# Kernel tuning notes

Hardware: AMD Instinct MI355X
Metric: run time of the kernel (lower is better)

## Reference

```python
import jax, jax.numpy as jnp
import numpy as np

CHEB_K = 3

def setup_inputs() -> dict:
    key = jax.random.key(0)
    ks = jax.random.split(key, 6)
    bs, node, in_dim, out_dim = 8, 1024, 64, 64
    d_e, t_d, embed_dim = 10, 6, 16
    return {
        "x": jax.random.normal(ks[0], (bs, node, in_dim), dtype=jnp.float32),
        "node_emb": jax.random.normal(ks[1], (node, d_e), dtype=jnp.float32),
        "t": jax.random.normal(ks[2], (bs, t_d), dtype=jnp.float32),
        "n_t": jax.random.normal(ks[3], (bs, t_d), dtype=jnp.float32),
        "p": jnp.zeros((1,), dtype=jnp.float32),
        "weights_pool": jax.random.normal(ks[4], (embed_dim, CHEB_K, in_dim, out_dim), dtype=jnp.float32),
        "bias_pool": jax.random.normal(ks[5], (embed_dim, out_dim), dtype=jnp.float32),
    }

def reference(x, node_emb, t, n_t, p, weights_pool, bias_pool):
    # x: [bs, node, in_dim]; node_emb: [node, d_e]; t, n_t: [bs, t_d]
    bs, node, _ = x.shape
    # static adjacency logits shared across batch: [node, node]
    a = node_emb @ node_emb.T
    # temporal scalar per batch: bmm of [bs,1,t_d] x [bs,t_d,1] -> [bs,1,1]
    a_t = jnp.einsum('bd,bd->b', n_t, t)[:, None, None]
    _a = a[None, :, :] + a_t                       # [bs, node, node]
    # period=False branch
    A = jax.nn.softmax(jax.nn.relu(_a), axis=2)    # [bs, node, node]
    # Chebyshev recursion: T0=I, T1=A, Tk = 2A@T_{k-1} - T_{k-2}
    I = jnp.broadcast_to(jnp.eye(node, dtype=x.dtype), (bs, node, node))
    supports = [I, A]
    for _ in range(2, CHEB_K):
        supports.append(jnp.matmul(2.0 * A, supports[-1]) - supports[-2])
    cheb = jnp.stack(supports, axis=1)             # [bs, k, node, node]
    # node+time embedding: [bs, node, d_e + t_d] = [bs, node, embed_dim]
    emb = jnp.concatenate(
        [jnp.broadcast_to(node_emb[None], (bs, node, node_emb.shape[1])),
         jnp.broadcast_to(n_t[:, None, :], (bs, node, n_t.shape[1]))], axis=-1)
    # graph conv: x_g[b,n,k,i] = sum_m cheb[b,k,n,m] x[b,m,i]
    x_g = jnp.einsum('bknm,bmc->bnkc', cheb, x)
    # fuse per-node weight generation into final contraction (same math as
    # weights = einsum('bnd,dkio->bnkio') followed by einsum('bnki,bnkio->bno'))
    out = jnp.einsum('bnki,bnd,dkio->bno', x_g, emb, weights_pool)
    bias = jnp.einsum('bnd,do->bno', emb, bias_pool)
    return out + bias
```

## Files before the change

### kernel.cpp

```cpp
#include <hip/hip_runtime.h>
#include <hip/hip_bf16.h>

#define NODE 1024
#define BS 8
#define XG_K 208

struct alignas(8) bf4 { __hip_bfloat16 a, b, c, d; };
typedef short short8 __attribute__((ext_vector_type(8)));
typedef float f32x16 __attribute__((ext_vector_type(16)));

__global__ __launch_bounds__(256) void k_attn(const float* __restrict__ ne,
                                              const float* __restrict__ t,
                                              const float* __restrict__ nt,
                                              __hip_bfloat16* __restrict__ A16) {
    __shared__ float nel[NODE * 11];
    int tid = threadIdx.x;
    int w = tid >> 6, lane = tid & 63;
    int n = (blockIdx.x << 2) + w;

    for (int i = tid; i < NODE * 10; i += 256) nel[(i / 10) * 11 + (i % 10)] = ne[i];

    float at[8];
#pragma unroll
    for (int b = 0; b < 8; ++b) {
        float s = 0.f;
#pragma unroll
        for (int j = 0; j < 6; ++j) s += nt[b * 6 + j] * t[b * 6 + j];
        at[b] = s;
    }
    __syncthreads();

    float nr[10];
#pragma unroll
    for (int d = 0; d < 10; ++d) nr[d] = nel[n * 11 + d];

    float v[16];
#pragma unroll
    for (int j = 0; j < 16; ++j) {
        const float* row = &nel[(lane + (j << 6)) * 11];
        float s = 0.f;
#pragma unroll
        for (int d = 0; d < 10; ++d) s += nr[d] * row[d];
        v[j] = s;
    }

#pragma unroll
    for (int b = 0; b < 8; ++b) {
        float u[16], s = 0.f;
#pragma unroll
        for (int j = 0; j < 16; ++j) {
            u[j] = __expf(fmaxf(v[j] + at[b], 0.f));
            s += u[j];
        }
#pragma unroll
        for (int off = 32; off > 0; off >>= 1) s += __shfl_xor(s, off);
        float inv = 1.f / s;
        __hip_bfloat16* dst = A16 + (((size_t)(b << 10) + n) << 10);
#pragma unroll
        for (int j = 0; j < 16; ++j) dst[lane + (j << 6)] = __float2bfloat16(u[j] * inv);
    }
}

__global__ __launch_bounds__(256) void k_prepw(const float* __restrict__ x,
                                               const float* __restrict__ W,
                                               const float* __restrict__ bp,
                                               __hip_bfloat16* __restrict__ xT,
                                               __hip_bfloat16* __restrict__ xg,
                                               __hip_bfloat16* __restrict__ wt) {
    __shared__ __hip_bfloat16 sh[64 * XG_K];
    int tid = threadIdx.x;

    if (blockIdx.x < 128) {
        typedef __hip_bfloat16 row72[72];
        row72* T = (row72*)sh;
        int b = blockIdx.x >> 4;
        int n0 = (blockIdx.x & 15) * 64;
        int nloc = tid >> 2, f0 = (tid & 3) * 16;
        size_t row = (size_t)(b << 10) + n0 + nloc;
        {
            const float* src = x + row * 64 + f0;
            __hip_bfloat16* dst = xg + row * XG_K + f0;
#pragma unroll
            for (int j = 0; j < 16; j += 4) {
                float4 vv = *(const float4*)(src + j);
                bf4 o;
                o.a = __float2bfloat16(vv.x); o.b = __float2bfloat16(vv.y);
                o.c = __float2bfloat16(vv.z); o.d = __float2bfloat16(vv.w);
                *(bf4*)(dst + j) = o;
                T[f0 + j][nloc] = o.a; T[f0 + j + 1][nloc] = o.b;
                T[f0 + j + 2][nloc] = o.c; T[f0 + j + 3][nloc] = o.d;
            }
        }
        if (tid < 64) {
            __hip_bfloat16* d2 = xg + ((size_t)(b << 10) + n0 + tid) * XG_K + 192;
            d2[0] = __float2bfloat16(1.0f);
#pragma unroll
            for (int j = 1; j < 16; ++j) d2[j] = __float2bfloat16(0.0f);
        }
        __syncthreads();
        {
            int f = tid >> 2, c0 = (tid & 3) * 16;
            __hip_bfloat16* dst = xT + ((size_t)b * 64 + f) * 1024 + n0 + c0;
#pragma unroll
            for (int j = 0; j < 16; ++j) dst[j] = T[f][c0 + j];
        }
    } else {
        int d = blockIdx.x - 128;
        const float* Wd = W + (size_t)d * 192 * 64;
        for (int i = tid; i < 192 * 64; i += 256) {
            int k = i >> 6, o = i & 63;
            sh[o * XG_K + k] = __float2bfloat16(Wd[i]);
        }
        if (tid < 64) {
            sh[tid * XG_K + 192] = __float2bfloat16(bp[d * 64 + tid]);
#pragma unroll
            for (int j = 1; j < 16; ++j) sh[tid * XG_K + 192 + j] = __float2bfloat16(0.0f);
        }
        __syncthreads();
        __hip_bfloat16* dst = wt + (size_t)d * 64 * XG_K;
        for (int i = tid; i < 64 * XG_K; i += 256) dst[i] = sh[i];
    }
}

#define LOADG(slot, g) do {                                                   \
    const __hip_bfloat16* qa = pa + (g) * 64;                                 \
    const __hip_bfloat16* qb = pb + (g) * 64;                                 \
    as[slot][0] = *(const short8*)(qa);      as[slot][1] = *(const short8*)(qa + 16); \
    as[slot][2] = *(const short8*)(qa + 32); as[slot][3] = *(const short8*)(qa + 48); \
    bs[slot][0] = *(const short8*)(qb);      bs[slot][1] = *(const short8*)(qb + 16); \
    bs[slot][2] = *(const short8*)(qb + 32); bs[slot][3] = *(const short8*)(qb + 48); \
} while (0)

template<bool FIRST>
__global__ __launch_bounds__(256) void k_spmm_mfma(const __hip_bfloat16* __restrict__ A16,
                                                   const __hip_bfloat16* __restrict__ srcT,
                                                   const float* __restrict__ xres,
                                                   __hip_bfloat16* __restrict__ xg,
                                                   __hip_bfloat16* __restrict__ youtT) {
    __shared__ float P[2][32][67];
    int b = blockIdx.x >> 5;
    int n0 = (blockIdx.x & 31) << 5;
    int tid = threadIdx.x;
    int wv = tid >> 6, lane = tid & 63;
    int fh = wv & 1, kh = wv >> 1;
    int l31 = lane & 31, hi = lane >> 5;

    const __hip_bfloat16* pa = srcT + ((size_t)b * 64 + fh * 32 + l31) * 1024 + (kh << 9) + hi * 8;
    const __hip_bfloat16* pb = A16 + ((size_t)b << 20) + (size_t)(n0 + l31) * 1024 + (kh << 9) + hi * 8;

    f32x16 acc0, acc1;
#pragma unroll
    for (int i = 0; i < 16; ++i) { acc0[i] = 0.f; acc1[i] = 0.f; }

    short8 as[3][4], bs[3][4];
    LOADG(0, 0);
    LOADG(1, 1);
#pragma unroll
    for (int g = 0; g < 8; ++g) {
        if (g + 2 < 8) { LOADG((g + 2) % 3, g + 2); }
        int cu = g % 3;
        acc0 = __builtin_amdgcn_mfma_f32_32x32x16_bf16(as[cu][0], bs[cu][0], acc0, 0, 0, 0);
        acc1 = __builtin_amdgcn_mfma_f32_32x32x16_bf16(as[cu][1], bs[cu][1], acc1, 0, 0, 0);
        acc0 = __builtin_amdgcn_mfma_f32_32x32x16_bf16(as[cu][2], bs[cu][2], acc0, 0, 0, 0);
        acc1 = __builtin_amdgcn_mfma_f32_32x32x16_bf16(as[cu][3], bs[cu][3], acc1, 0, 0, 0);
    }
#pragma unroll
    for (int i = 0; i < 16; ++i) acc0[i] += acc1[i];

    if (kh == 1) {
#pragma unroll
        for (int r = 0; r < 16; ++r) {
            int f = hi * 4 + (r >> 2) * 8 + (r & 3);
            P[fh][l31][f] = acc0[r];
        }
    }
    __syncthreads();
    if (kh == 0) {
#pragma unroll
        for (int r = 0; r < 16; ++r) {
            int f = hi * 4 + (r >> 2) * 8 + (r & 3);
            acc0[r] += P[fh][l31][f];
        }

        int node = n0 + l31;
        size_t row = (size_t)(b << 10) + node;
        const int base = FIRST ? 64 : 128;
#pragma unroll
        for (int rg = 0; rg < 4; ++rg) {
            int fb = fh * 32 + hi * 4 + rg * 8;
            float vx = acc0[rg * 4], vy = acc0[rg * 4 + 1];
            float vz = acc0[rg * 4 + 2], vw = acc0[rg * 4 + 3];
            if (!FIRST) {
                float4 xv = *(const float4*)(xres + row * 64 + fb);
                vx = 2.f * vx - xv.x; vy = 2.f * vy - xv.y;
                vz = 2.f * vz - xv.z; vw = 2.f * vw - xv.w;
            }
            bf4 o;
            o.a = __float2bfloat16(vx); o.b = __float2bfloat16(vy);
            o.c = __float2bfloat16(vz); o.d = __float2bfloat16(vw);
            *(bf4*)(xg + row * XG_K + base + fb) = o;
        }
        if (FIRST) {
#pragma unroll
            for (int r = 0; r < 16; ++r) {
                int f = fh * 32 + hi * 4 + (r >> 2) * 8 + (r & 3);
                youtT[((size_t)b * 64 + f) * 1024 + node] = __float2bfloat16(acc0[r]);
            }
        }
    }
}

__global__ __launch_bounds__(512) void k_fuse(const __hip_bfloat16* __restrict__ xg,
                                              const __hip_bfloat16* __restrict__ wt,
                                              const float* __restrict__ ne,
                                              const float* __restrict__ nt,
                                              float* __restrict__ out) {
    __shared__ float P[8][32][67];
    int m0 = blockIdx.x * 32;
    int tid = threadIdx.x;
    int w = tid >> 6;
    int lane = tid & 63;
    int l31 = lane & 31, hi = lane >> 5;
    int b = m0 >> 10;
    int n = (m0 & 1023) + l31;

    int d0 = 2 * w, d1 = 2 * w + 1;
    float e0 = (d0 < 10) ? ne[n * 10 + d0] : nt[b * 6 + (d0 - 10)];
    float e1 = (d1 < 10) ? ne[n * 10 + d1] : nt[b * 6 + (d1 - 10)];

    short8 xf[13];
    const __hip_bfloat16* px = xg + (size_t)(m0 + l31) * XG_K + hi * 8;
#pragma unroll
    for (int k = 0; k < 13; ++k) xf[k] = *(const short8*)(px + k * 16);

    f32x16 z00, z01, z10, z11;
#pragma unroll
    for (int i = 0; i < 16; ++i) { z00[i] = 0.f; z01[i] = 0.f; z10[i] = 0.f; z11[i] = 0.f; }

    const __hip_bfloat16* pw0 = wt + ((size_t)d0 * 64 + l31) * XG_K + hi * 8;
    const __hip_bfloat16* pw1 = pw0 + (size_t)64 * XG_K;
#pragma unroll
    for (int k = 0; k < 13; ++k) {
        short8 a00 = *(const short8*)(pw0 + k * 16);
        short8 a01 = *(const short8*)(pw0 + (size_t)32 * XG_K + k * 16);
        short8 a10 = *(const short8*)(pw1 + k * 16);
        short8 a11 = *(const short8*)(pw1 + (size_t)32 * XG_K + k * 16);
        z00 = __builtin_amdgcn_mfma_f32_32x32x16_bf16(a00, xf[k], z00, 0, 0, 0);
        z01 = __builtin_amdgcn_mfma_f32_32x32x16_bf16(a01, xf[k], z01, 0, 0, 0);
        z10 = __builtin_amdgcn_mfma_f32_32x32x16_bf16(a10, xf[k], z10, 0, 0, 0);
        z11 = __builtin_amdgcn_mfma_f32_32x32x16_bf16(a11, xf[k], z11, 0, 0, 0);
    }

#pragma unroll
    for (int r = 0; r < 16; ++r) {
        int o = (r & 3) + 8 * (r >> 2) + 4 * hi;
        P[w][l31][o]      = e0 * z00[r] + e1 * z10[r];
        P[w][l31][o + 32] = e0 * z01[r] + e1 * z11[r];
    }
    __syncthreads();

    int m = tid >> 4, o0 = (tid & 15) * 4;
    float s0 = 0.f, s1 = 0.f, s2 = 0.f, s3 = 0.f;
#pragma unroll
    for (int ww = 0; ww < 8; ++ww) {
        s0 += P[ww][m][o0];
        s1 += P[ww][m][o0 + 1];
        s2 += P[ww][m][o0 + 2];
        s3 += P[ww][m][o0 + 3];
    }
    *(float4*)(out + (size_t)(m0 + m) * 64 + o0) = make_float4(s0, s1, s2, s3);
}

extern "C" void kernel_launch(void* const* d_in, const int* in_sizes, int n_in,
                              void* d_out, int out_size, void* d_ws, size_t ws_size,
                              hipStream_t stream) {
    const float* x  = (const float*)d_in[0];
    const float* ne = (const float*)d_in[1];
    const float* t  = (const float*)d_in[2];
    const float* nt = (const float*)d_in[3];
    const float* W  = (const float*)d_in[5];
    const float* bp = (const float*)d_in[6];
    float* out = (float*)d_out;

    __hip_bfloat16* wsb = (__hip_bfloat16*)d_ws;
    __hip_bfloat16* A16 = wsb;
    __hip_bfloat16* xT  = wsb + 8388608;
    __hip_bfloat16* y1T = wsb + 8912896;
    __hip_bfloat16* xg  = wsb + 9437184;
    __hip_bfloat16* wt  = wsb + 11141120;

    k_attn<<<NODE / 4, 256, 0, stream>>>(ne, t, nt, A16);
    k_prepw<<<144, 256, 0, stream>>>(x, W, bp, xT, xg, wt);
    k_spmm_mfma<true ><<<BS * 32, 256, 0, stream>>>(A16, xT,  x, xg, y1T);
    k_spmm_mfma<false><<<BS * 32, 256, 0, stream>>>(A16, y1T, x, xg, nullptr);
    k_fuse<<<BS * (NODE / 32), 512, 0, stream>>>(xg, wt, ne, nt, out);
}
```

Measured before the change: 117.2 us.

## Store intermediates in MFMA fragment-major layout for contiguous operand loads

All workspace buffers (attention matrix, transposed x, y1, xg, packed weights) are now written in a fragment-tiled layout. Each wave's short8 MFMA operand loads become fully contiguous 512-byte chunks instead of strided row reads. The attention kernel is reorganized to one batch per block with 512 threads, where each thread computes 64 columns and the row sum is reduced through shared memory. This trades more complex index math and scattered 2-byte y1 stores for coalesced loads in the GEMM kernels.

Result: slower. 123.4 us (+5.3%).

```diff
diff --git a/kernel.cpp b/kernel.cpp
--- a/kernel.cpp
+++ b/kernel.cpp
@@ -3,150 +3,187 @@
 
 #define NODE 1024
 #define BS 8
-#define XG_K 208
 
 struct alignas(8) bf4 { __hip_bfloat16 a, b, c, d; };
 typedef short short8 __attribute__((ext_vector_type(8)));
 typedef float f32x16 __attribute__((ext_vector_type(16)));
 
-__global__ __launch_bounds__(256) void k_attn(const float* __restrict__ ne,
+__device__ __forceinline__ short bf16bits(float f) {
+    __hip_bfloat16 h = __float2bfloat16(f);
+    return *reinterpret_cast<short*>(&h);
+}
+__device__ __forceinline__ float bitstofl(short s) {
+    unsigned u = ((unsigned)(unsigned short)s) << 16;
+    return __uint_as_float(u);
+}
+
+
+__global__ __launch_bounds__(512) void k_attn(const float* __restrict__ ne,
                                               const float* __restrict__ t,
                                               const float* __restrict__ nt,
-                                              __hip_bfloat16* __restrict__ A16) {
+                                              __hip_bfloat16* __restrict__ A16f) {
     __shared__ float nel[NODE * 11];
+    __shared__ float ssum[8][32];
     int tid = threadIdx.x;
     int w = tid >> 6, lane = tid & 63;
-    int n = (blockIdx.x << 2) + w;
-
-    for (int i = tid; i < NODE * 10; i += 256) nel[(i / 10) * 11 + (i % 10)] = ne[i];
-
-    float at[8];
-#pragma unroll
-    for (int b = 0; b < 8; ++b) {
+    int l31 = lane & 31, hi = lane >> 5;
+    int bidx = blockIdx.x;
+    int b = bidx >> 5;
+    int n = (bidx & 31) * 32 + l31;
+
+    for (int i = tid; i < NODE * 10; i += 512) nel[(i / 10) * 11 + (i % 10)] = ne[i];
+
+    float at = 0.f;
+#pragma unroll
+    for (int j = 0; j < 6; ++j) at += nt[b * 6 + j] * t[b * 6 + j];
+    __syncthreads();
+
+    float nr[10];
+#pragma unroll
+    for (int d = 0; d < 10; ++d) nr[d] = nel[n * 11 + d];
+
+    int mbase = w * 128 + hi * 64;
+    float z[64];
+#pragma unroll
+    for (int m = 0; m < 64; ++m) {
+        const float* row = &nel[(mbase + m) * 11];
         float s = 0.f;
 #pragma unroll
-        for (int j = 0; j < 6; ++j) s += nt[b * 6 + j] * t[b * 6 + j];
-        at[b] = s;
-    }
+        for (int d = 0; d < 10; ++d) s += nr[d] * row[d];
+        z[m] = s;
+    }
+
+    short8 u16[8];
+    float s = 0.f;
+#pragma unroll
+    for (int c = 0; c < 8; ++c) {
+        short8 pk;
+#pragma unroll
+        for (int j = 0; j < 8; ++j) {
+            float u = __expf(fmaxf(z[c * 8 + j] + at, 0.f));
+            s += u;
+            pk[j] = bf16bits(u);
+        }
+        u16[c] = pk;
+    }
+    s += __shfl_xor(s, 32);
+    if (hi == 0) ssum[w][l31] = s;
     __syncthreads();
-
-    float nr[10];
-#pragma unroll
-    for (int d = 0; d < 10; ++d) nr[d] = nel[n * 11 + d];
-
-    float v[16];
-#pragma unroll
-    for (int j = 0; j < 16; ++j) {
-        const float* row = &nel[(lane + (j << 6)) * 11];
-        float s = 0.f;
-#pragma unroll
-        for (int d = 0; d < 10; ++d) s += nr[d] * row[d];
-        v[j] = s;
-    }
-
-#pragma unroll
-    for (int b = 0; b < 8; ++b) {
-        float u[16], s = 0.f;
-#pragma unroll
-        for (int j = 0; j < 16; ++j) {
-            u[j] = __expf(fmaxf(v[j] + at[b], 0.f));
-            s += u[j];
-        }
-#pragma unroll
-        for (int off = 32; off > 0; off >>= 1) s += __shfl_xor(s, off);
-        float inv = 1.f / s;
-        __hip_bfloat16* dst = A16 + (((size_t)(b << 10) + n) << 10);
-#pragma unroll
-        for (int j = 0; j < 16; ++j) dst[lane + (j << 6)] = __float2bfloat16(u[j] * inv);
+    float tot = 0.f;
+#pragma unroll
+    for (int ww = 0; ww < 8; ++ww) tot += ssum[ww][l31];
+    float inv = 1.f / tot;
+
+    __hip_bfloat16* base = A16f + ((size_t)(bidx * 64 + w * 8 + hi * 4) * 2) * 256 + l31 * 8;
+#pragma unroll
+    for (int c = 0; c < 8; ++c) {
+        short8 pk = u16[c];
+        short8 o;
+#pragma unroll
+        for (int j = 0; j < 8; ++j) o[j] = bf16bits(bitstofl(pk[j]) * inv);
+        *(short8*)(base + c * 256) = o;
     }
 }
 
 __global__ __launch_bounds__(256) void k_prepw(const float* __restrict__ x,
                                                const float* __restrict__ W,
                                                const float* __restrict__ bp,
-                                               __hip_bfloat16* __restrict__ xT,
-                                               __hip_bfloat16* __restrict__ xg,
-                                               __hip_bfloat16* __restrict__ wt) {
-    __shared__ __hip_bfloat16 sh[64 * XG_K];
+                                               __hip_bfloat16* __restrict__ xTf,
+                                               __hip_bfloat16* __restrict__ xgf,
+                                               __hip_bfloat16* __restrict__ wtf) {
     int tid = threadIdx.x;
-
     if (blockIdx.x < 128) {
-        typedef __hip_bfloat16 row72[72];
-        row72* T = (row72*)sh;
+        __shared__ __hip_bfloat16 T[64][72];
         int b = blockIdx.x >> 4;
         int n0 = (blockIdx.x & 15) * 64;
-        int nloc = tid >> 2, f0 = (tid & 3) * 16;
-        size_t row = (size_t)(b << 10) + n0 + nloc;
-        {
-            const float* src = x + row * 64 + f0;
-            __hip_bfloat16* dst = xg + row * XG_K + f0;
-#pragma unroll
-            for (int j = 0; j < 16; j += 4) {
-                float4 vv = *(const float4*)(src + j);
-                bf4 o;
-                o.a = __float2bfloat16(vv.x); o.b = __float2bfloat16(vv.y);
-                o.c = __float2bfloat16(vv.z); o.d = __float2bfloat16(vv.w);
-                *(bf4*)(dst + j) = o;
-                T[f0 + j][nloc] = o.a; T[f0 + j + 1][nloc] = o.b;
-                T[f0 + j + 2][nloc] = o.c; T[f0 + j + 3][nloc] = o.d;
-            }
-        }
-        if (tid < 64) {
-            __hip_bfloat16* d2 = xg + ((size_t)(b << 10) + n0 + tid) * XG_K + 192;
-            d2[0] = __float2bfloat16(1.0f);
-#pragma unroll
-            for (int j = 1; j < 16; ++j) d2[j] = __float2bfloat16(0.0f);
+#pragma unroll
+        for (int it = 0; it < 2; ++it) {
+            int i = it * 256 + tid;
+            int l31 = i & 31, hi2 = (i >> 5) & 1, ks = (i >> 6) & 3, rt = i >> 8;
+            int node = n0 + rt * 32 + l31;
+            const float* src = x + ((size_t)b * 1024 + node) * 64 + ks * 16 + hi2 * 8;
+            short8 o;
+#pragma unroll
+            for (int j = 0; j < 8; ++j) o[j] = bf16bits(src[j]);
+            size_t rtg = (size_t)b * 32 + (n0 >> 5) + rt;
+            *(short8*)(xgf + (rtg * 13 + ks) * 512 + hi2 * 256 + l31 * 8) = o;
+#pragma unroll
+            for (int j = 0; j < 8; ++j) {
+                __hip_bfloat16 h;
+                *reinterpret_cast<short*>(&h) = o[j];
+                T[ks * 16 + hi2 * 8 + j][rt * 32 + l31] = h;
+            }
+        }
+        for (int i = tid; i < 1024; i += 256) {
+            int rt = i >> 9, e = i & 511;
+            size_t rtg = (size_t)b * 32 + (n0 >> 5) + rt;
+            float val = ((e & 7) == 0 && e < 256) ? 1.0f : 0.0f;
+            xgf[(rtg * 13 + 12) * 512 + e] = __float2bfloat16(val);
         }
         __syncthreads();
-        {
-            int f = tid >> 2, c0 = (tid & 3) * 16;
-            __hip_bfloat16* dst = xT + ((size_t)b * 64 + f) * 1024 + n0 + c0;
-#pragma unroll
-            for (int j = 0; j < 16; ++j) dst[j] = T[f][c0 + j];
+#pragma unroll
+        for (int fh = 0; fh < 2; ++fh) {
+            int f = fh * 32 + (tid & 31);
+            int m8 = tid >> 5;
+            int m = n0 + m8 * 8;
+            short8 o;
+#pragma unroll
+            for (int j = 0; j < 8; ++j) {
+                __hip_bfloat16 h = T[f][m8 * 8 + j];
+                o[j] = *reinterpret_cast<short*>(&h);
+            }
+            size_t addr = (((size_t)(b * 2 + fh) * 64 + (m >> 4)) * 2 + ((m >> 3) & 1)) * 256 + (f & 31) * 8;
+            *(short8*)(xTf + addr) = o;
         }
     } else {
         int d = blockIdx.x - 128;
         const float* Wd = W + (size_t)d * 192 * 64;
-        for (int i = tid; i < 192 * 64; i += 256) {
-            int k = i >> 6, o = i & 63;
-            sh[o * XG_K + k] = __float2bfloat16(Wd[i]);
-        }
-        if (tid < 64) {
-            sh[tid * XG_K + 192] = __float2bfloat16(bp[d * 64 + tid]);
-#pragma unroll
-            for (int j = 1; j < 16; ++j) sh[tid * XG_K + 192 + j] = __float2bfloat16(0.0f);
-        }
-        __syncthreads();
-        __hip_bfloat16* dst = wt + (size_t)d * 64 * XG_K;
-        for (int i = tid; i < 64 * XG_K; i += 256) dst[i] = sh[i];
+        for (int i = tid; i < 1664; i += 256) {
+            int l31 = i & 31, hi2 = (i >> 5) & 1;
+            int ks = (i >> 6) % 13, oh = (i >> 6) / 13;
+            int o = oh * 32 + l31;
+            short8 v;
+#pragma unroll
+            for (int j = 0; j < 8; ++j) {
+                int k = ks * 16 + hi2 * 8 + j;
+                float f = (k < 192) ? Wd[(size_t)k * 64 + o]
+                                    : ((k == 192) ? bp[d * 64 + o] : 0.0f);
+                v[j] = bf16bits(f);
+            }
+            size_t addr = ((((size_t)d * 2 + oh) * 13 + ks) * 2 + hi2) * 256 + l31 * 8;
+            *(short8*)(wtf + addr) = v;
+        }
     }
 }
 
 #define LOADG(slot, g) do {                                                   \
-    const __hip_bfloat16* qa = pa + (g) * 64;                                 \
-    const __hip_bfloat16* qb = pb + (g) * 64;                                 \
-    as[slot][0] = *(const short8*)(qa);      as[slot][1] = *(const short8*)(qa + 16); \
-    as[slot][2] = *(const short8*)(qa + 32); as[slot][3] = *(const short8*)(qa + 48); \
-    bs[slot][0] = *(const short8*)(qb);      bs[slot][1] = *(const short8*)(qb + 16); \
-    bs[slot][2] = *(const short8*)(qb + 32); bs[slot][3] = *(const short8*)(qb + 48); \
+    as[slot][0] = *(const short8*)(pa + ((g) * 4 + 0) * 512);                 \
+    as[slot][1] = *(const short8*)(pa + ((g) * 4 + 1) * 512);                 \
+    as[slot][2] = *(const short8*)(pa + ((g) * 4 + 2) * 512);                 \
+    as[slot][3] = *(const short8*)(pa + ((g) * 4 + 3) * 512);                 \
+    bs[slot][0] = *(const short8*)(pb + ((g) * 4 + 0) * 512);                 \
+    bs[slot][1] = *(const short8*)(pb + ((g) * 4 + 1) * 512);                 \
+    bs[slot][2] = *(const short8*)(pb + ((g) * 4 + 2) * 512);                 \
+    bs[slot][3] = *(const short8*)(pb + ((g) * 4 + 3) * 512);                 \
 } while (0)
 
 template<bool FIRST>
-__global__ __launch_bounds__(256) void k_spmm_mfma(const __hip_bfloat16* __restrict__ A16,
-                                                   const __hip_bfloat16* __restrict__ srcT,
+__global__ __launch_bounds__(256) void k_spmm_mfma(const __hip_bfloat16* __restrict__ A16f,
+                                                   const __hip_bfloat16* __restrict__ srcTf,
                                                    const float* __restrict__ xres,
-                                                   __hip_bfloat16* __restrict__ xg,
-                                                   __hip_bfloat16* __restrict__ youtT) {
+                                                   __hip_bfloat16* __restrict__ xgf,
+                                                   __hip_bfloat16* __restrict__ y1Tf) {
     __shared__ float P[2][32][67];
     int b = blockIdx.x >> 5;
-    int n0 = (blockIdx.x & 31) << 5;
+    int ntile = blockIdx.x & 31;
+    int n0 = ntile << 5;
     int tid = threadIdx.x;
     int wv = tid >> 6, lane = tid & 63;
     int fh = wv & 1, kh = wv >> 1;
     int l31 = lane & 31, hi = lane >> 5;
 
-    const __hip_bfloat16* pa = srcT + ((size_t)b * 64 + fh * 32 + l31) * 1024 + (kh << 9) + hi * 8;
-    const __hip_bfloat16* pb = A16 + ((size_t)b << 20) + (size_t)(n0 + l31) * 1024 + (kh << 9) + hi * 8;
+    const __hip_bfloat16* pa = srcTf + (((size_t)(b * 2 + fh) * 64 + kh * 32) * 2 + hi) * 256 + l31 * 8;
+    const __hip_bfloat16* pb = A16f + (((size_t)(b * 32 + ntile) * 64 + kh * 32) * 2 + hi) * 256 + l31 * 8;
 
     f32x16 acc0, acc1;
 #pragma unroll
@@ -184,7 +221,7 @@
 
         int node = n0 + l31;
         size_t row = (size_t)(b << 10) + node;
-        const int base = FIRST ? 64 : 128;
+        size_t rtg = (size_t)b * 32 + ntile;
 #pragma unroll
         for (int rg = 0; rg < 4; ++rg) {
             int fb = fh * 32 + hi * 4 + rg * 8;
@@ -198,25 +235,31 @@
             bf4 o;
             o.a = __float2bfloat16(vx); o.b = __float2bfloat16(vy);
             o.c = __float2bfloat16(vz); o.d = __float2bfloat16(vw);
-            *(bf4*)(xg + row * XG_K + base + fb) = o;
+            int kstep = (FIRST ? 4 : 8) + fh * 2 + (rg >> 1);
+            int hi2 = rg & 1;
+            *(bf4*)(xgf + (rtg * 13 + kstep) * 512 + hi2 * 256 + l31 * 8 + hi * 4) = o;
         }
         if (FIRST) {
 #pragma unroll
             for (int r = 0; r < 16; ++r) {
                 int f = fh * 32 + hi * 4 + (r >> 2) * 8 + (r & 3);
-                youtT[((size_t)b * 64 + f) * 1024 + node] = __float2bfloat16(acc0[r]);
-            }
-        }
-    }
-}
-
-__global__ __launch_bounds__(512) void k_fuse(const __hip_bfloat16* __restrict__ xg,
-                                              const __hip_bfloat16* __restrict__ wt,
+                size_t addr = (((size_t)(b * 2 + fh) * 64 + ((n0 + l31) >> 4)) * 2 + ((l31 >> 3) & 1)) * 256
+                              + (f & 31) * 8 + (l31 & 7);
+                __hip_bfloat16 h = __float2bfloat16(acc0[r]);
+                y1Tf[addr] = h;
+            }
+        }
+    }
+}
+
+__global__ __launch_bounds__(512) void k_fuse(const __hip_bfloat16* __restrict__ xgf,
+                                              const __hip_bfloat16* __restrict__ wtf,
                                               const float* __restrict__ ne,
                                               const float* __restrict__ nt,
                                               float* __restrict__ out) {
     __shared__ float P[8][32][67];
-    int m0 = blockIdx.x * 32;
+    int rt = blockIdx.x;
+    int m0 = rt * 32;
     int tid = threadIdx.x;
     int w = tid >> 6;
     int lane = tid & 63;
@@ -229,22 +272,21 @@
     float e1 = (d1 < 10) ? ne[n * 10 + d1] : nt[b * 6 + (d1 - 10)];
 
     short8 xf[13];
-    const __hip_bfloat16* px = xg + (size_t)(m0 + l31) * XG_K + hi * 8;
-#pragma unroll
-    for (int k = 0; k < 13; ++k) xf[k] = *(const short8*)(px + k * 16);
+    const __hip_bfloat16* px = xgf + (size_t)rt * 6656 + hi * 256 + l31 * 8;
+#pragma unroll
+    for (int k = 0; k < 13; ++k) xf[k] = *(const short8*)(px + k * 512);
 
     f32x16 z00, z01, z10, z11;
 #pragma unroll
     for (int i = 0; i < 16; ++i) { z00[i] = 0.f; z01[i] = 0.f; z10[i] = 0.f; z11[i] = 0.f; }
 
-    const __hip_bfloat16* pw0 = wt + ((size_t)d0 * 64 + l31) * XG_K + hi * 8;
-    const __hip_bfloat16* pw1 = pw0 + (size_t)64 * XG_K;
+    const __hip_bfloat16* pw0 = wtf + (size_t)d0 * 13312 + hi * 256 + l31 * 8;
 #pragma unroll
     for (int k = 0; k < 13; ++k) {
-        short8 a00 = *(const short8*)(pw0 + k * 16);
-        short8 a01 = *(const short8*)(pw0 + (size_t)32 * XG_K + k * 16);
-        short8 a10 = *(const short8*)(pw1 + k * 16);
-        short8 a11 = *(const short8*)(pw1 + (size_t)32 * XG_K + k * 16);
+        short8 a00 = *(const short8*)(pw0 + k * 512);
+        short8 a01 = *(const short8*)(pw0 + 6656 + k * 512);
+        short8 a10 = *(const short8*)(pw0 + 13312 + k * 512);
+        short8 a11 = *(const short8*)(pw0 + 13312 + 6656 + k * 512);
         z00 = __builtin_amdgcn_mfma_f32_32x32x16_bf16(a00, xf[k], z00, 0, 0, 0);
         z01 = __builtin_amdgcn_mfma_f32_32x32x16_bf16(a01, xf[k], z01, 0, 0, 0);
         z10 = __builtin_amdgcn_mfma_f32_32x32x16_bf16(a10, xf[k], z10, 0, 0, 0);
@@ -283,15 +325,15 @@
     float* out = (float*)d_out;
 
     __hip_bfloat16* wsb = (__hip_bfloat16*)d_ws;
-    __hip_bfloat16* A16 = wsb;
-    __hip_bfloat16* xT  = wsb + 8388608;
-    __hip_bfloat16* y1T = wsb + 8912896;
-    __hip_bfloat16* xg  = wsb + 9437184;
-    __hip_bfloat16* wt  = wsb + 11141120;
-
-    k_attn<<<NODE / 4, 256, 0, stream>>>(ne, t, nt, A16);
-    k_prepw<<<144, 256, 0, stream>>>(x, W, bp, xT, xg, wt);
-    k_spmm_mfma<true ><<<BS * 32, 256, 0, stream>>>(A16, xT,  x, xg, y1T);
-    k_spmm_mfma<false><<<BS * 32, 256, 0, stream>>>(A16, y1T, x, xg, nullptr);
-    k_fuse<<<BS * (NODE / 32), 512, 0, stream>>>(xg, wt, ne, nt, out);
-}
+    __hip_bfloat16* A16f = wsb;
+    __hip_bfloat16* xTf  = wsb + 8388608;
+    __hip_bfloat16* y1Tf = wsb + 8912896;
+    __hip_bfloat16* xgf  = wsb + 9437184;
+    __hip_bfloat16* wtf  = wsb + 11141120;
+
+    k_attn<<<BS * 32, 512, 0, stream>>>(ne, t, nt, A16f);
+    k_prepw<<<144, 256, 0, stream>>>(x, W, bp, xTf, xgf, wtf);
+    k_spmm_mfma<true ><<<BS * 32, 256, 0, stream>>>(A16f, xTf,  x, xgf, y1Tf);
+    k_spmm_mfma<false><<<BS * 32, 256, 0, stream>>>(A16f, y1Tf, x, xgf, nullptr);
+    k_fuse<<<BS * (NODE / 32), 512, 0, stream>>>(xgf, wtf, ne, nt, out);
+}
```

## Merge front kernels and fuse second Chebyshev step into final contraction

Applied to the files above, without the earlier changes.

Combines the attention softmax, x conversion and weight-prep kernels into one launch, and fuses the second Chebyshev SpMM with the per-node weight contraction so T2·x stays in shared memory instead of going through global xg. It also precomputes the time-embedding part of the weights per batch (wb), cutting the final contraction from eight weight-slice waves to six. The aim is fewer launches and less global traffic, at the cost of a heavier fused kernel with only 256 blocks and a larger shared-memory footprint.

After: 121.5 us. 1.04x slower.

```diff
diff --git a/kernel.cpp b/kernel.cpp
--- a/kernel.cpp
+++ b/kernel.cpp
@@ -9,72 +9,78 @@
 typedef short short8 __attribute__((ext_vector_type(8)));
 typedef float f32x16 __attribute__((ext_vector_type(16)));
 
-__global__ __launch_bounds__(256) void k_attn(const float* __restrict__ ne,
-                                              const float* __restrict__ t,
-                                              const float* __restrict__ nt,
-                                              __hip_bfloat16* __restrict__ A16) {
-    __shared__ float nel[NODE * 11];
-    int tid = threadIdx.x;
-    int w = tid >> 6, lane = tid & 63;
-    int n = (blockIdx.x << 2) + w;
-
-    for (int i = tid; i < NODE * 10; i += 256) nel[(i / 10) * 11 + (i % 10)] = ne[i];
-
-    float at[8];
-#pragma unroll
-    for (int b = 0; b < 8; ++b) {
-        float s = 0.f;
-#pragma unroll
-        for (int j = 0; j < 6; ++j) s += nt[b * 6 + j] * t[b * 6 + j];
-        at[b] = s;
-    }
-    __syncthreads();
-
-    float nr[10];
-#pragma unroll
-    for (int d = 0; d < 10; ++d) nr[d] = nel[n * 11 + d];
-
-    float v[16];
-#pragma unroll
-    for (int j = 0; j < 16; ++j) {
-        const float* row = &nel[(lane + (j << 6)) * 11];
-        float s = 0.f;
-#pragma unroll
-        for (int d = 0; d < 10; ++d) s += nr[d] * row[d];
-        v[j] = s;
-    }
-
-#pragma unroll
-    for (int b = 0; b < 8; ++b) {
-        float u[16], s = 0.f;
-#pragma unroll
-        for (int j = 0; j < 16; ++j) {
-            u[j] = __expf(fmaxf(v[j] + at[b], 0.f));
-            s += u[j];
-        }
-#pragma unroll
-        for (int off = 32; off > 0; off >>= 1) s += __shfl_xor(s, off);
-        float inv = 1.f / s;
-        __hip_bfloat16* dst = A16 + (((size_t)(b << 10) + n) << 10);
-#pragma unroll
-        for (int j = 0; j < 16; ++j) dst[lane + (j << 6)] = __float2bfloat16(u[j] * inv);
-    }
-}
-
-__global__ __launch_bounds__(256) void k_prepw(const float* __restrict__ x,
+__device__ __forceinline__ short bf16bits(float f) {
+    __hip_bfloat16 h = __float2bfloat16(f);
+    return *reinterpret_cast<short*>(&h);
+}
+
+__global__ __launch_bounds__(256) void k_front(const float* __restrict__ ne,
+                                               const float* __restrict__ t,
+                                               const float* __restrict__ nt,
+                                               const float* __restrict__ x,
                                                const float* __restrict__ W,
                                                const float* __restrict__ bp,
+                                               __hip_bfloat16* __restrict__ A16,
                                                __hip_bfloat16* __restrict__ xT,
                                                __hip_bfloat16* __restrict__ xg,
-                                               __hip_bfloat16* __restrict__ wt) {
-    __shared__ __hip_bfloat16 sh[64 * XG_K];
+                                               __hip_bfloat16* __restrict__ wt,
+                                               __hip_bfloat16* __restrict__ wb) {
+    __shared__ __align__(16) char shbuf[45056];
+    int bidx = blockIdx.x;
     int tid = threadIdx.x;
 
-    if (blockIdx.x < 128) {
+    if (bidx < 256) {
+        float* nel = (float*)shbuf;
+        int w = tid >> 6, lane = tid & 63;
+        int n = (bidx << 2) + w;
+
+        for (int i = tid; i < NODE * 10; i += 256) nel[(i / 10) * 11 + (i % 10)] = ne[i];
+
+        float at[8];
+#pragma unroll
+        for (int b = 0; b < 8; ++b) {
+            float s = 0.f;
+#pragma unroll
+            for (int j = 0; j < 6; ++j) s += nt[b * 6 + j] * t[b * 6 + j];
+            at[b] = s;
+        }
+        __syncthreads();
+
+        float nr[10];
+#pragma unroll
+        for (int d = 0; d < 10; ++d) nr[d] = nel[n * 11 + d];
+
+        float v[16];
+#pragma unroll
+        for (int j = 0; j < 16; ++j) {
+            const float* row = &nel[(lane + (j << 6)) * 11];
+            float s = 0.f;
+#pragma unroll
+            for (int d = 0; d < 10; ++d) s += nr[d] * row[d];
+            v[j] = s;
+        }
+
+#pragma unroll
+        for (int b = 0; b < 8; ++b) {
+            float u[16], s = 0.f;
+#pragma unroll
+            for (int j = 0; j < 16; ++j) {
+                u[j] = __expf(fmaxf(v[j] + at[b], 0.f));
+                s += u[j];
+            }
+#pragma unroll
+            for (int off = 32; off > 0; off >>= 1) s += __shfl_xor(s, off);
+            float inv = 1.f / s;
+            __hip_bfloat16* dst = A16 + (((size_t)(b << 10) + n) << 10);
+#pragma unroll
+            for (int j = 0; j < 16; ++j) dst[lane + (j << 6)] = __float2bfloat16(u[j] * inv);
+        }
+    } else if (bidx < 384) {
         typedef __hip_bfloat16 row72[72];
-        row72* T = (row72*)sh;
-        int b = blockIdx.x >> 4;
-        int n0 = (blockIdx.x & 15) * 64;
+        row72* T = (row72*)shbuf;
+        int bx = bidx - 256;
+        int b = bx >> 4;
+        int n0 = (bx & 15) * 64;
         int nloc = tid >> 2, f0 = (tid & 3) * 16;
         size_t row = (size_t)(b << 10) + n0 + nloc;
         {
@@ -104,21 +110,38 @@
 #pragma unroll
             for (int j = 0; j < 16; ++j) dst[j] = T[f][c0 + j];
         }
+    } else if (bidx < 400) {
+        int d = bidx - 384;
+        const float* Wd = W + (size_t)d * 192 * 64;
+        __hip_bfloat16* dst = wt + (size_t)d * 64 * XG_K;
+        for (int i = tid; i < 64 * XG_K; i += 256) {
+            int o = i / XG_K, k = i % XG_K;
+            float f = (k < 192) ? Wd[(size_t)k * 64 + o]
+                                : ((k == 192) ? bp[d * 64 + o] : 0.0f);
+            dst[i] = __float2bfloat16(f);
+        }
     } else {
-        int d = blockIdx.x - 128;
-        const float* Wd = W + (size_t)d * 192 * 64;
-        for (int i = tid; i < 192 * 64; i += 256) {
-            int k = i >> 6, o = i & 63;
-            sh[o * XG_K + k] = __float2bfloat16(Wd[i]);
-        }
-        if (tid < 64) {
-            sh[tid * XG_K + 192] = __float2bfloat16(bp[d * 64 + tid]);
-#pragma unroll
-            for (int j = 1; j < 16; ++j) sh[tid * XG_K + 192 + j] = __float2bfloat16(0.0f);
-        }
-        __syncthreads();
-        __hip_bfloat16* dst = wt + (size_t)d * 64 * XG_K;
-        for (int i = tid; i < 64 * XG_K; i += 256) dst[i] = sh[i];
+        int idx = bidx - 400;
+        int b = idx >> 1, oh = idx & 1;
+        float ntl[6];
+#pragma unroll
+        for (int dd = 0; dd < 6; ++dd) ntl[dd] = nt[b * 6 + dd];
+        __hip_bfloat16* dst = wb + (size_t)b * 64 * XG_K + oh * 32 * XG_K;
+        for (int i = tid; i < 32 * XG_K; i += 256) {
+            int ol = i / XG_K, k = i % XG_K;
+            int o = oh * 32 + ol;
+            float s = 0.f;
+            if (k < 192) {
+#pragma unroll
+                for (int dd = 0; dd < 6; ++dd)
+                    s += ntl[dd] * W[((size_t)(10 + dd) * 192 + k) * 64 + o];
+            } else if (k == 192) {
+#pragma unroll
+                for (int dd = 0; dd < 6; ++dd)
+                    s += ntl[dd] * bp[(10 + dd) * 64 + o];
+            }
+            dst[i] = __float2bfloat16(s);
+        }
     }
 }
 
@@ -131,12 +154,10 @@
     bs[slot][2] = *(const short8*)(qb + 32); bs[slot][3] = *(const short8*)(qb + 48); \
 } while (0)
 
-template<bool FIRST>
-__global__ __launch_bounds__(256) void k_spmm_mfma(const __hip_bfloat16* __restrict__ A16,
-                                                   const __hip_bfloat16* __restrict__ srcT,
-                                                   const float* __restrict__ xres,
-                                                   __hip_bfloat16* __restrict__ xg,
-                                                   __hip_bfloat16* __restrict__ youtT) {
+__global__ __launch_bounds__(256) void k_spmm1(const __hip_bfloat16* __restrict__ A16,
+                                               const __hip_bfloat16* __restrict__ xT,
+                                               __hip_bfloat16* __restrict__ xg,
+                                               __hip_bfloat16* __restrict__ y1T) {
     __shared__ float P[2][32][67];
     int b = blockIdx.x >> 5;
     int n0 = (blockIdx.x & 31) << 5;
@@ -145,7 +166,7 @@
     int fh = wv & 1, kh = wv >> 1;
     int l31 = lane & 31, hi = lane >> 5;
 
-    const __hip_bfloat16* pa = srcT + ((size_t)b * 64 + fh * 32 + l31) * 1024 + (kh << 9) + hi * 8;
+    const __hip_bfloat16* pa = xT + ((size_t)b * 64 + fh * 32 + l31) * 1024 + (kh << 9) + hi * 8;
     const __hip_bfloat16* pb = A16 + ((size_t)b << 20) + (size_t)(n0 + l31) * 1024 + (kh << 9) + hi * 8;
 
     f32x16 acc0, acc1;
@@ -169,106 +190,166 @@
 
     if (kh == 1) {
 #pragma unroll
-        for (int r = 0; r < 16; ++r) {
-            int f = hi * 4 + (r >> 2) * 8 + (r & 3);
-            P[fh][l31][f] = acc0[r];
-        }
+        for (int r = 0; r < 16; ++r)
+            P[fh][l31][hi * 4 + (r >> 2) * 8 + (r & 3)] = acc0[r];
     }
     __syncthreads();
     if (kh == 0) {
 #pragma unroll
-        for (int r = 0; r < 16; ++r) {
-            int f = hi * 4 + (r >> 2) * 8 + (r & 3);
-            acc0[r] += P[fh][l31][f];
-        }
+        for (int r = 0; r < 16; ++r)
+            acc0[r] += P[fh][l31][hi * 4 + (r >> 2) * 8 + (r & 3)];
 
         int node = n0 + l31;
         size_t row = (size_t)(b << 10) + node;
-        const int base = FIRST ? 64 : 128;
 #pragma unroll
         for (int rg = 0; rg < 4; ++rg) {
             int fb = fh * 32 + hi * 4 + rg * 8;
-            float vx = acc0[rg * 4], vy = acc0[rg * 4 + 1];
-            float vz = acc0[rg * 4 + 2], vw = acc0[rg * 4 + 3];
-            if (!FIRST) {
-                float4 xv = *(const float4*)(xres + row * 64 + fb);
-                vx = 2.f * vx - xv.x; vy = 2.f * vy - xv.y;
-                vz = 2.f * vz - xv.z; vw = 2.f * vw - xv.w;
-            }
             bf4 o;
-            o.a = __float2bfloat16(vx); o.b = __float2bfloat16(vy);
-            o.c = __float2bfloat16(vz); o.d = __float2bfloat16(vw);
-            *(bf4*)(xg + row * XG_K + base + fb) = o;
-        }
-        if (FIRST) {
+            o.a = __float2bfloat16(acc0[rg * 4]);
+            o.b = __float2bfloat16(acc0[rg * 4 + 1]);
+            o.c = __float2bfloat16(acc0[rg * 4 + 2]);
+            o.d = __float2bfloat16(acc0[rg * 4 + 3]);
+            *(bf4*)(xg + row * XG_K + 64 + fb) = o;
+        }
+#pragma unroll
+        for (int r = 0; r < 16; ++r) {
+            int f = fh * 32 + hi * 4 + (r >> 2) * 8 + (r & 3);
+            y1T[((size_t)b * 64 + f) * 1024 + node] = __float2bfloat16(acc0[r]);
+        }
+    }
+}
+
+__global__ __launch_bounds__(512) void k_sf(const __hip_bfloat16* __restrict__ A16,
+                                            const __hip_bfloat16* __restrict__ y1T,
+                                            const float* __restrict__ x,
+                                            const __hip_bfloat16* __restrict__ xg,
+                                            const __hip_bfloat16* __restrict__ wt,
+                                            const __hip_bfloat16* __restrict__ wb,
+                                            const float* __restrict__ ne,
+                                            float* __restrict__ out) {
+    __shared__ __align__(16) char buf[51456];
+    __shared__ __hip_bfloat16 Y2[32][66];
+    typedef float p3_t[2][32][33];
+    p3_t* P = (p3_t*)buf;
+    typedef float pf_t[32][67];
+    pf_t* PF = (pf_t*)buf;
+
+    int bidx = blockIdx.x;
+    int b = bidx >> 5, ntile = bidx & 31;
+    int n0 = ntile << 5;
+    int tid = threadIdx.x;
+    int w = tid >> 6, lane = tid & 63;
+    int l31 = lane & 31, hi = lane >> 5;
+
+    {
+        int fh = w & 1, kq = w >> 1;
+        const __hip_bfloat16* pa = y1T + ((size_t)b * 64 + fh * 32 + l31) * 1024 + kq * 256 + hi * 8;
+        const __hip_bfloat16* pb = A16 + ((size_t)b << 20) + (size_t)(n0 + l31) * 1024 + kq * 256 + hi * 8;
+
+        f32x16 a0, a1;
+#pragma unroll
+        for (int i = 0; i < 16; ++i) { a0[i] = 0.f; a1[i] = 0.f; }
+#pragma unroll
+        for (int gi = 0; gi < 16; gi += 2) {
+            short8 av0 = *(const short8*)(pa + gi * 16);
+            short8 bv0 = *(const short8*)(pb + gi * 16);
+            short8 av1 = *(const short8*)(pa + gi * 16 + 16);
+            short8 bv1 = *(const short8*)(pb + gi * 16 + 16);
+            a0 = __builtin_amdgcn_mfma_f32_32x32x16_bf16(av0, bv0, a0, 0, 0, 0);
+            a1 = __builtin_amdgcn_mfma_f32_32x32x16_bf16(av1, bv1, a1, 0, 0, 0);
+        }
+#pragma unroll
+        for (int i = 0; i < 16; ++i) a0[i] += a1[i];
+
+        if (kq != 0) {
+#pragma unroll
+            for (int r = 0; r < 16; ++r)
+                P[kq - 1][fh][l31][hi * 4 + (r >> 2) * 8 + (r & 3)] = a0[r];
+        }
+        __syncthreads();
+        if (kq == 0) {
 #pragma unroll
             for (int r = 0; r < 16; ++r) {
-                int f = fh * 32 + hi * 4 + (r >> 2) * 8 + (r & 3);
-                youtT[((size_t)b * 64 + f) * 1024 + node] = __float2bfloat16(acc0[r]);
-            }
-        }
-    }
-}
-
-__global__ __launch_bounds__(512) void k_fuse(const __hip_bfloat16* __restrict__ xg,
-                                              const __hip_bfloat16* __restrict__ wt,
-                                              const float* __restrict__ ne,
-                                              const float* __restrict__ nt,
-                                              float* __restrict__ out) {
-    __shared__ float P[8][32][67];
-    int m0 = blockIdx.x * 32;
-    int tid = threadIdx.x;
-    int w = tid >> 6;
-    int lane = tid & 63;
-    int l31 = lane & 31, hi = lane >> 5;
-    int b = m0 >> 10;
-    int n = (m0 & 1023) + l31;
-
-    int d0 = 2 * w, d1 = 2 * w + 1;
-    float e0 = (d0 < 10) ? ne[n * 10 + d0] : nt[b * 6 + (d0 - 10)];
-    float e1 = (d1 < 10) ? ne[n * 10 + d1] : nt[b * 6 + (d1 - 10)];
-
-    short8 xf[13];
-    const __hip_bfloat16* px = xg + (size_t)(m0 + l31) * XG_K + hi * 8;
-#pragma unroll
-    for (int k = 0; k < 13; ++k) xf[k] = *(const short8*)(px + k * 16);
-
-    f32x16 z00, z01, z10, z11;
-#pragma unroll
-    for (int i = 0; i < 16; ++i) { z00[i] = 0.f; z01[i] = 0.f; z10[i] = 0.f; z11[i] = 0.f; }
-
-    const __hip_bfloat16* pw0 = wt + ((size_t)d0 * 64 + l31) * XG_K + hi * 8;
-    const __hip_bfloat16* pw1 = pw0 + (size_t)64 * XG_K;
-#pragma unroll
-    for (int k = 0; k < 13; ++k) {
-        short8 a00 = *(const short8*)(pw0 + k * 16);
-        short8 a01 = *(const short8*)(pw0 + (size_t)32 * XG_K + k * 16);
-        short8 a10 = *(const short8*)(pw1 + k * 16);
-        short8 a11 = *(const short8*)(pw1 + (size_t)32 * XG_K + k * 16);
-        z00 = __builtin_amdgcn_mfma_f32_32x32x16_bf16(a00, xf[k], z00, 0, 0, 0);
-        z01 = __builtin_amdgcn_mfma_f32_32x32x16_bf16(a01, xf[k], z01, 0, 0, 0);
-        z10 = __builtin_amdgcn_mfma_f32_32x32x16_bf16(a10, xf[k], z10, 0, 0, 0);
-        z11 = __builtin_amdgcn_mfma_f32_32x32x16_bf16(a11, xf[k], z11, 0, 0, 0);
-    }
-
-#pragma unroll
-    for (int r = 0; r < 16; ++r) {
-        int o = (r & 3) + 8 * (r >> 2) + 4 * hi;
-        P[w][l31][o]      = e0 * z00[r] + e1 * z10[r];
-        P[w][l31][o + 32] = e0 * z01[r] + e1 * z11[r];
+                int f = hi * 4 + (r >> 2) * 8 + (r & 3);
+                a0[r] += P[0][fh][l31][f] + P[1][fh][l31][f] + P[2][fh][l31][f];
+            }
+            size_t row = (size_t)(b << 10) + n0 + l31;
+#pragma unroll
+            for (int rg = 0; rg < 4; ++rg) {
+                int fb = fh * 32 + hi * 4 + rg * 8;
+                float4 xv = *(const float4*)(x + row * 64 + fb);
+                bf4 o;
+                o.a = __float2bfloat16(2.f * a0[rg * 4]     - xv.x);
+                o.b = __float2bfloat16(2.f * a0[rg * 4 + 1] - xv.y);
+                o.c = __float2bfloat16(2.f * a0[rg * 4 + 2] - xv.z);
+                o.d = __float2bfloat16(2.f * a0[rg * 4 + 3] - xv.w);
+                *(bf4*)(&Y2[l31][fb]) = o;
+            }
+        }
+    }
+    __syncthreads();
+
+    if (w < 6) {
+        int n = n0 + l31;
+        int s0 = 2 * w, s1 = 2 * w + 1;
+        float e0, e1;
+        const __hip_bfloat16 *base0, *base1;
+        if (w < 5) {
+            e0 = ne[n * 10 + s0];
+            e1 = ne[n * 10 + s1];
+            base0 = wt + ((size_t)s0 * 64 + l31) * XG_K + hi * 8;
+            base1 = wt + ((size_t)s1 * 64 + l31) * XG_K + hi * 8;
+        } else {
+            e0 = 1.0f;
+            e1 = 0.0f;
+            base0 = wb + ((size_t)b * 64 + l31) * XG_K + hi * 8;
+            base1 = base0;
+        }
+
+        short8 xf[13];
+        const __hip_bfloat16* px = xg + ((size_t)(bidx * 32) + l31) * XG_K + hi * 8;
+#pragma unroll
+        for (int wk = 0; wk < 13; ++wk) {
+            if (wk >= 8 && wk < 12)
+                xf[wk] = *(const short8*)(&Y2[l31][(wk - 8) * 16 + hi * 8]);
+            else
+                xf[wk] = *(const short8*)(px + wk * 16);
+        }
+
+        f32x16 z00, z01, z10, z11;
+#pragma unroll
+        for (int i = 0; i < 16; ++i) { z00[i] = 0.f; z01[i] = 0.f; z10[i] = 0.f; z11[i] = 0.f; }
+
+#pragma unroll
+        for (int wk = 0; wk < 13; ++wk) {
+            short8 a00 = *(const short8*)(base0 + wk * 16);
+            short8 a01 = *(const short8*)(base0 + (size_t)32 * XG_K + wk * 16);
+            short8 a10 = *(const short8*)(base1 + wk * 16);
+            short8 a11 = *(const short8*)(base1 + (size_t)32 * XG_K + wk * 16);
+            z00 = __builtin_amdgcn_mfma_f32_32x32x16_bf16(a00, xf[wk], z00, 0, 0, 0);
+            z01 = __builtin_amdgcn_mfma_f32_32x32x16_bf16(a01, xf[wk], z01, 0, 0, 0);
+            z10 = __builtin_amdgcn_mfma_f32_32x32x16_bf16(a10, xf[wk], z10, 0, 0, 0);
+            z11 = __builtin_amdgcn_mfma_f32_32x32x16_bf16(a11, xf[wk], z11, 0, 0, 0);
+        }
+#pragma unroll
+        for (int r = 0; r < 16; ++r) {
+            int o = (r & 3) + 8 * (r >> 2) + 4 * hi;
+            PF[w][l31][o]      = e0 * z00[r] + e1 * z10[r];
+            PF[w][l31][o + 32] = e0 * z01[r] + e1 * z11[r];
+        }
     }
     __syncthreads();
 
     int m = tid >> 4, o0 = (tid & 15) * 4;
     float s0 = 0.f, s1 = 0.f, s2 = 0.f, s3 = 0.f;
 #pragma unroll
-    for (int ww = 0; ww < 8; ++ww) {
-        s0 += P[ww][m][o0];
-        s1 += P[ww][m][o0 + 1];
-        s2 += P[ww][m][o0 + 2];
-        s3 += P[ww][m][o0 + 3];
-    }
-    *(float4*)(out + (size_t)(m0 + m) * 64 + o0) = make_float4(s0, s1, s2, s3);
+    for (int ww = 0; ww < 6; ++ww) {
+        s0 += PF[ww][m][o0];
+        s1 += PF[ww][m][o0 + 1];
+        s2 += PF[ww][m][o0 + 2];
+        s3 += PF[ww][m][o0 + 3];
+    }
+    *(float4*)(out + ((size_t)(bidx * 32) + m) * 64 + o0) = make_float4(s0, s1, s2, s3);
 }
 
 extern "C" void kernel_launch(void* const* d_in, const int* in_sizes, int n_in,
@@ -288,10 +369,9 @@
     __hip_bfloat16* y1T = wsb + 8912896;
     __hip_bfloat16* xg  = wsb + 9437184;
     __hip_bfloat16* wt  = wsb + 11141120;
-
-    k_attn<<<NODE / 4, 256, 0, stream>>>(ne, t, nt, A16);
-    k_prepw<<<144, 256, 0, stream>>>(x, W, bp, xT, xg, wt);
-    k_spmm_mfma<true ><<<BS * 32, 256, 0, stream>>>(A16, xT,  x, xg, y1T);
-    k_spmm_mfma<false><<<BS * 32, 256, 0, stream>>>(A16, y1T, x, xg, nullptr);
-    k_fuse<<<BS * (NODE / 32), 512, 0, stream>>>(xg, wt, ne, nt, out);
-}
+    __hip_bfloat16* wb  = wsb + 11354112;
+
+    k_front<<<416, 256, 0, stream>>>(ne, t, nt, x, W, bp, A16, xT, xg, wt, wb);
+    k_spmm1<<<BS * 32, 256, 0, stream>>>(A16, xT, xg, y1T);
+    k_sf<<<BS * 32, 512, 0, stream>>>(A16, y1T, x, xg, wt, wb, ne, out);
+}
```
